# Kernel tuning notes

Measured on AMD Instinct MI355X. Metric: run time of the kernel, lower is better.

Reference implementation:

```python
import jax, jax.numpy as jnp
import numpy as np

BN_EPS = 1e-5


def setup_inputs() -> dict:
    key = jax.random.key(0)
    k1, k2, k3, k4 = jax.random.split(key, 4)
    N_IN, N_OUT, K, M, C_IN, C_OUT = 500000, 125000, 27, 60000, 64, 64
    x = jax.random.normal(k1, (N_IN, C_IN), dtype=jnp.float32)
    # Per-offset conv weights, fan-in scaled like Minkowski's kaiming init
    W = jax.random.normal(k2, (K, C_IN, C_OUT), dtype=jnp.float32) * (1.0 / np.sqrt(K * C_IN))
    gamma = jnp.ones((C_OUT,), dtype=jnp.float32)
    beta = jnp.zeros((C_OUT,), dtype=jnp.float32)
    # Kernel map: for each of the 27 offsets, M (input_idx, output_idx) pairs
    in_idx = jax.random.randint(k3, (K, M), 0, N_IN, dtype=jnp.int64)
    out_idx = jax.random.randint(k4, (K, M), 0, N_OUT, dtype=jnp.int64)
    return {"x": x, "W": W, "gamma": gamma, "beta": beta,
            "in_idx": in_idx, "out_idx": out_idx, "n_out": 125000}


def reference(x, W, gamma, beta, in_idx, out_idx, n_out):
    # Sparse 3D conv via kernel map: gather -> per-offset GEMM -> scatter-add.
    C_out = W.shape[-1]
    gathered = x[in_idx]                                   # [K, M, C_in]
    contrib = jnp.einsum('kmc,kcd->kmd', gathered, W)      # [K, M, C_out]
    out = jnp.zeros((n_out, C_out), dtype=x.dtype)
    out = out.at[out_idx.reshape(-1)].add(contrib.reshape(-1, C_out))  # [N_out, C_out]
    # MinkowskiBatchNorm (training mode): per-channel batch stats over all points
    mean = jnp.mean(out, axis=0)
    var = jnp.mean(jnp.square(out - mean), axis=0)         # biased variance
    y = (out - mean) * jax.lax.rsqrt(var + BN_EPS) * gamma + beta
    return y
```

## Files before the change

kernel.cpp:

```cpp
#include <hip/hip_runtime.h>

typedef __attribute__((ext_vector_type(8))) short short8;
typedef __attribute__((ext_vector_type(4))) float f32x4;

#define K_OFF    27
#define M_PAIRS  60000
#define C_DIM    64
#define N_IN     500000
#define N_OUT_C  125000
#define BN_EPS   1e-5f
#define E_TOT    (K_OFF * M_PAIRS)

#define TILES_PER_K  ((M_PAIRS + 63) / 64)
#define TOTAL_WT     (K_OFF * TILES_PER_K)

#define CONTRIB_BYTES ((size_t)E_TOT * C_DIM * 2)
#define WT_OFF    CONTRIB_BYTES
#define WT_BYTES  ((size_t)K_OFF * C_DIM * C_DIM * 2)
#define CNT_OFF   (WT_OFF + WT_BYTES)
#define CNT_BYTES ((size_t)N_OUT_C * 4)
#define OFF_OFF   (CNT_OFF + CNT_BYTES)
#define CUR_OFF   (OFF_OFF + CNT_BYTES)
#define BSUM_OFF  (CUR_OFF + CNT_BYTES)
#define ST_OFF    (BSUM_OFF + 4096)
#define XB_OFF    ((ST_OFF + 512 + 255) & ~(size_t)255)
#define XB_BYTES  ((size_t)N_IN * C_DIM * 2)
#define WS_MID    XB_OFF
#define WS_FULL   (XB_OFF + XB_BYTES)

#define SCAN_BS 256
#define SCAN_NB ((N_OUT_C + SCAN_BS - 1) / SCAN_BS)

#define PREP_XBLK 2048
#define PREP_WBLK ((K_OFF * C_DIM * C_DIM + 255) / 256)
#define PREP_HBLK 1024

__device__ __forceinline__ unsigned short f32_to_bf16(float f) {
    unsigned u = __float_as_uint(f);
    u += 0x7FFFu + ((u >> 16) & 1u);
    return (unsigned short)(u >> 16);
}
__device__ __forceinline__ float bf16f(unsigned short u) {
    return __uint_as_float((unsigned)u << 16);
}

__global__ __launch_bounds__(256) void prep(
    const float* __restrict__ x, unsigned short* __restrict__ xb,
    const float* __restrict__ W, unsigned short* __restrict__ wt,
    const int* __restrict__ out_idx, unsigned* __restrict__ cnt, int nx)
{
    int b = blockIdx.x;
    if (b < nx) {
        const int tid = b * 256 + threadIdx.x;
        const int T   = nx * 256;
        const int n4  = N_IN * C_DIM / 4;
        const float4* x4 = (const float4*)x;
        ushort4* b4 = (ushort4*)xb;
        for (int i = tid; i < n4; i += T) {
            float4 v = x4[i];
            ushort4 o;
            o.x = f32_to_bf16(v.x); o.y = f32_to_bf16(v.y);
            o.z = f32_to_bf16(v.z); o.w = f32_to_bf16(v.w);
            b4[i] = o;
        }
        return;
    }
    b -= nx;
    if (b < PREP_WBLK) {
        const int tid = b * 256 + threadIdx.x;
        if (tid < K_OFF * C_DIM * C_DIM) {
            const int c = tid & 63;
            const int d = (tid >> 6) & 63;
            const int k = tid >> 12;
            wt[tid] = f32_to_bf16(W[(k << 12) + (c << 6) + d]);
        }
        return;
    }
    b -= PREP_WBLK;
    for (int e = b * 256 + threadIdx.x; e < E_TOT; e += PREP_HBLK * 256)
        atomicAdd(&cnt[out_idx[e]], 1u);
}

__global__ __launch_bounds__(SCAN_BS) void scan_a(const unsigned* __restrict__ cnt,
                                                  unsigned* __restrict__ off,
                                                  unsigned* __restrict__ bsum) {
    __shared__ unsigned s[SCAN_BS];
    const int idx = blockIdx.x * SCAN_BS + threadIdx.x;
    const unsigned v = (idx < N_OUT_C) ? cnt[idx] : 0u;
    s[threadIdx.x] = v;
    __syncthreads();
    for (int d = 1; d < SCAN_BS; d <<= 1) {
        unsigned t = (threadIdx.x >= d) ? s[threadIdx.x - d] : 0u;
        __syncthreads();
        s[threadIdx.x] += t;
        __syncthreads();
    }
    if (idx < N_OUT_C) off[idx] = s[threadIdx.x] - v;
    if (threadIdx.x == SCAN_BS - 1) bsum[blockIdx.x] = s[threadIdx.x];
}

__global__ __launch_bounds__(512) void scan_b(unsigned* __restrict__ bsum) {
    __shared__ unsigned s[512];
    const unsigned v = (threadIdx.x < SCAN_NB) ? bsum[threadIdx.x] : 0u;
    s[threadIdx.x] = v;
    __syncthreads();
    for (int d = 1; d < 512; d <<= 1) {
        unsigned t = (threadIdx.x >= d) ? s[threadIdx.x - d] : 0u;
        __syncthreads();
        s[threadIdx.x] += t;
        __syncthreads();
    }
    if (threadIdx.x < SCAN_NB) bsum[threadIdx.x] = s[threadIdx.x] - v;
}

__global__ __launch_bounds__(SCAN_BS) void scan_c(unsigned* __restrict__ off,
                                                  unsigned* __restrict__ cur,
                                                  const unsigned* __restrict__ bsum) {
    const int idx = blockIdx.x * SCAN_BS + threadIdx.x;
    if (idx < N_OUT_C) {
        const unsigned o = off[idx] + bsum[blockIdx.x];
        off[idx] = o;
        cur[idx] = o;
    }
}

template<bool BF16G>
__global__ __launch_bounds__(256, 4) void mfma_contrib(
    const float* __restrict__ x, const unsigned short* __restrict__ xb,
    const unsigned short* __restrict__ wt,
    const int* __restrict__ in_idx, const int* __restrict__ out_idx,
    unsigned* __restrict__ cursor, unsigned short* __restrict__ contrib)
{
    const int gwave = blockIdx.x * 4 + (threadIdx.x >> 6);
    if (gwave >= TOTAL_WT) return;
    const int lane = threadIdx.x & 63;
    const int lg = lane >> 4;
    const int lr = lane & 15;

    const int k  = gwave / TILES_PER_K;
    const int t  = gwave % TILES_PER_K;
    const int m0 = t * 64;
    const int kbase = k * M_PAIRS;

    short8 bfr[2][4];
    const unsigned short* wtk = wt + (size_t)k * C_DIM * C_DIM;
#pragma unroll
    for (int ks = 0; ks < 2; ++ks)
#pragma unroll
        for (int ct = 0; ct < 4; ++ct)
            bfr[ks][ct] = *(const short8*)(wtk + (ct * 16 + lr) * C_DIM + ks * 32 + lg * 8);

    int pos = -1;
    {
        const int mrow = m0 + lane;
        if (mrow < M_PAIRS)
            pos = (int)atomicAdd(&cursor[out_idx[kbase + mrow]], 1u);
    }

    int aidx[4];
#pragma unroll
    for (int rt = 0; rt < 4; ++rt) {
        const int m = m0 + rt * 16 + lr;
        aidx[rt] = (m < M_PAIRS) ? in_idx[kbase + m] : -1;
    }

    f32x4 acc[4][4] = {};
#pragma unroll
    for (int ks = 0; ks < 2; ++ks) {
#pragma unroll
        for (int rt = 0; rt < 4; ++rt) {
            short8 a = {};
            if (aidx[rt] >= 0) {
                if constexpr (BF16G) {
                    a = *(const short8*)(xb + (size_t)aidx[rt] * C_DIM + ks * 32 + lg * 8);
                } else {
                    const float* xr = x + (size_t)aidx[rt] * C_DIM + ks * 32 + lg * 8;
                    float4 f0 = *(const float4*)xr;
                    float4 f1 = *(const float4*)(xr + 4);
                    a[0] = (short)f32_to_bf16(f0.x); a[1] = (short)f32_to_bf16(f0.y);
                    a[2] = (short)f32_to_bf16(f0.z); a[3] = (short)f32_to_bf16(f0.w);
                    a[4] = (short)f32_to_bf16(f1.x); a[5] = (short)f32_to_bf16(f1.y);
                    a[6] = (short)f32_to_bf16(f1.z); a[7] = (short)f32_to_bf16(f1.w);
                }
            }
#pragma unroll
            for (int ct = 0; ct < 4; ++ct)
                acc[rt][ct] = __builtin_amdgcn_mfma_f32_16x16x32_bf16(
                    a, bfr[ks][ct], acc[rt][ct], 0, 0, 0);
        }
    }

#pragma unroll
    for (int rt = 0; rt < 4; ++rt) {
#pragma unroll
        for (int j = 0; j < 4; ++j) {
            const int r = rt * 16 + lg * 4 + j;
            const int p = __shfl(pos, r);
            if (p >= 0) {
                unsigned short* dst = contrib + (size_t)p * C_DIM + lr;
#pragma unroll
                for (int ct = 0; ct < 4; ++ct)
                    dst[ct * 16] = f32_to_bf16(acc[rt][ct][j]);
            }
        }
    }
}

__global__ __launch_bounds__(256) void reduce_bn(
    const unsigned short* __restrict__ contrib, const unsigned* __restrict__ off,
    const unsigned* __restrict__ cnt, float* __restrict__ out,
    float* __restrict__ stats)
{
    __shared__ float ls[128];
    if (threadIdx.x < 128) ls[threadIdx.x] = 0.f;
    __syncthreads();
    const int lane = threadIdx.x & 63;
    const int lg = lane >> 4;
    const int lr = lane & 15;
    const int wid  = blockIdx.x * 4 + (threadIdx.x >> 6);
    const int NW   = gridDim.x * 4;
    const int span = (N_OUT_C + NW - 1) / NW;
    const int o0 = wid * span;
    const int o1 = (o0 + span < N_OUT_C) ? o0 + span : N_OUT_C;

    float ts0 = 0, ts1 = 0, ts2 = 0, ts3 = 0;
    float tq0 = 0, tq1 = 0, tq2 = 0, tq3 = 0;
    for (int o = o0; o < o1; ++o) {
        const unsigned base = off[o];
        const int n = (int)cnt[o];
        float s0 = 0, s1 = 0, s2 = 0, s3 = 0;
        for (int i = lg; i < n; i += 4) {
            const ushort4 u = *(const ushort4*)(
                contrib + ((size_t)base + i) * C_DIM + lr * 4);
            s0 += bf16f(u.x); s1 += bf16f(u.y);
            s2 += bf16f(u.z); s3 += bf16f(u.w);
        }
        s0 += __shfl_xor(s0, 16); s1 += __shfl_xor(s1, 16);
        s2 += __shfl_xor(s2, 16); s3 += __shfl_xor(s3, 16);
        s0 += __shfl_xor(s0, 32); s1 += __shfl_xor(s1, 32);
        s2 += __shfl_xor(s2, 32); s3 += __shfl_xor(s3, 32);
        if (lg == 0) {
            *(float4*)(out + (size_t)o * C_DIM + lr * 4) =
                make_float4(s0, s1, s2, s3);
            ts0 += s0; tq0 = fmaf(s0, s0, tq0);
            ts1 += s1; tq1 = fmaf(s1, s1, tq1);
            ts2 += s2; tq2 = fmaf(s2, s2, tq2);
            ts3 += s3; tq3 = fmaf(s3, s3, tq3);
        }
    }
    if (lg == 0) {
        atomicAdd(&ls[lr * 4 + 0], ts0); atomicAdd(&ls[lr * 4 + 1], ts1);
        atomicAdd(&ls[lr * 4 + 2], ts2); atomicAdd(&ls[lr * 4 + 3], ts3);
        atomicAdd(&ls[64 + lr * 4 + 0], tq0); atomicAdd(&ls[64 + lr * 4 + 1], tq1);
        atomicAdd(&ls[64 + lr * 4 + 2], tq2); atomicAdd(&ls[64 + lr * 4 + 3], tq3);
    }
    __syncthreads();
    if (threadIdx.x < 128) unsafeAtomicAdd(&stats[threadIdx.x], ls[threadIdx.x]);
}

__global__ __launch_bounds__(256) void bn_apply_f32(
    float* __restrict__ out, const float* __restrict__ stats,
    const float* __restrict__ gamma, const float* __restrict__ beta)
{
    __shared__ float ssc[C_DIM], ssh[C_DIM];
    if (threadIdx.x < C_DIM) {
        const float inv_n = 1.0f / (float)N_OUT_C;
        float mean = stats[threadIdx.x] * inv_n;
        float var  = stats[C_DIM + threadIdx.x] * inv_n - mean * mean;
        float inv  = rsqrtf(var + BN_EPS);
        float s    = inv * gamma[threadIdx.x];
        ssc[threadIdx.x] = s;
        ssh[threadIdx.x] = beta[threadIdx.x] - mean * s;
    }
    __syncthreads();
    const int tid = blockIdx.x * blockDim.x + threadIdx.x;
    const int T   = gridDim.x * blockDim.x;
    const int cq  = (tid & 15) * 4;
    const int total4 = N_OUT_C * C_DIM / 4;
    const float4 sc = make_float4(ssc[cq], ssc[cq+1], ssc[cq+2], ssc[cq+3]);
    const float4 sh = make_float4(ssh[cq], ssh[cq+1], ssh[cq+2], ssh[cq+3]);
    float4* o4 = (float4*)out;
    for (int i = tid; i < total4; i += T) {
        float4 v = o4[i];
        v.x = fmaf(v.x, sc.x, sh.x);
        v.y = fmaf(v.y, sc.y, sh.y);
        v.z = fmaf(v.z, sc.z, sh.z);
        v.w = fmaf(v.w, sc.w, sh.w);
        o4[i] = v;
    }
}

#define FCHUNKS  37
#define FWPK     (FCHUNKS * 4)
#define FSPAN    ((M_PAIRS + FWPK - 1) / FWPK)

__global__ __launch_bounds__(256, 4) void conv_scatter(
    const float* __restrict__ x, const float* __restrict__ W,
    const int* __restrict__ in_idx, const int* __restrict__ out_idx,
    float* __restrict__ out)
{
    const int k     = blockIdx.x / FCHUNKS;
    const int chunk = blockIdx.x % FCHUNKS;
    const int wid   = chunk * 4 + (threadIdx.x >> 6);
    const int lane  = threadIdx.x & 63;
    float wcol[C_DIM];
    const float* Wk = W + (size_t)k * C_DIM * C_DIM;
#pragma unroll
    for (int c = 0; c < C_DIM; ++c) wcol[c] = Wk[c * C_DIM + lane];
    const int kbase = k * M_PAIRS;
    const int m0 = wid * FSPAN;
    const int m1 = (m0 + FSPAN < M_PAIRS) ? m0 + FSPAN : M_PAIRS;
    for (int m = m0; m < m1; ++m) {
        int ii = __builtin_amdgcn_readfirstlane(in_idx[kbase + m]);
        int oi = __builtin_amdgcn_readfirstlane(out_idx[kbase + m]);
        const float* xr = x + (size_t)ii * C_DIM;
        float a0=0.f,a1=0.f,a2=0.f,a3=0.f;
#pragma unroll
        for (int c = 0; c < C_DIM; c += 4) {
            a0 = fmaf(xr[c+0], wcol[c+0], a0);
            a1 = fmaf(xr[c+1], wcol[c+1], a1);
            a2 = fmaf(xr[c+2], wcol[c+2], a2);
            a3 = fmaf(xr[c+3], wcol[c+3], a3);
        }
        unsafeAtomicAdd(out + (size_t)oi * C_DIM + lane, (a0+a1)+(a2+a3));
    }
}

__global__ __launch_bounds__(256) void bn_stats_f32(
    const float* __restrict__ acc, float* __restrict__ stats)
{
    const int tid = blockIdx.x * blockDim.x + threadIdx.x;
    const int T   = gridDim.x * blockDim.x;
    const int cq  = (tid & 15) * 4;
    const int total4 = N_OUT_C * C_DIM / 4;
    float s0=0,s1=0,s2=0,s3=0,q0=0,q1=0,q2=0,q3=0;
    const float4* a4 = (const float4*)acc;
    for (int i = tid; i < total4; i += T) {
        float4 v = a4[i];
        s0+=v.x; q0=fmaf(v.x,v.x,q0);
        s1+=v.y; q1=fmaf(v.y,v.y,q1);
        s2+=v.z; q2=fmaf(v.z,v.z,q2);
        s3+=v.w; q3=fmaf(v.w,v.w,q3);
    }
    __shared__ float ls[128];
    if (threadIdx.x < 128) ls[threadIdx.x] = 0.f;
    __syncthreads();
    atomicAdd(&ls[cq+0],s0); atomicAdd(&ls[cq+1],s1);
    atomicAdd(&ls[cq+2],s2); atomicAdd(&ls[cq+3],s3);
    atomicAdd(&ls[64+cq+0],q0); atomicAdd(&ls[64+cq+1],q1);
    atomicAdd(&ls[64+cq+2],q2); atomicAdd(&ls[64+cq+3],q3);
    __syncthreads();
    if (threadIdx.x < 128) unsafeAtomicAdd(&stats[threadIdx.x], ls[threadIdx.x]);
}

extern "C" void kernel_launch(void* const* d_in, const int* in_sizes, int n_in,
                              void* d_out, int out_size, void* d_ws, size_t ws_size,
                              hipStream_t stream)
{
    const float* x       = (const float*)d_in[0];
    const float* W       = (const float*)d_in[1];
    const float* gamma   = (const float*)d_in[2];
    const float* beta    = (const float*)d_in[3];
    const int*   in_idx  = (const int*)d_in[4];
    const int*   out_idx = (const int*)d_in[5];
    float* out = (float*)d_out;

    if (ws_size >= WS_MID) {
        unsigned short* contrib = (unsigned short*)d_ws;
        unsigned short* wt      = (unsigned short*)((char*)d_ws + WT_OFF);
        unsigned* cnt           = (unsigned*)((char*)d_ws + CNT_OFF);
        unsigned* off           = (unsigned*)((char*)d_ws + OFF_OFF);
        unsigned* cur           = (unsigned*)((char*)d_ws + CUR_OFF);
        unsigned* bsum          = (unsigned*)((char*)d_ws + BSUM_OFF);
        float* stats            = (float*)((char*)d_ws + ST_OFF);
        unsigned short* xb      = (unsigned short*)((char*)d_ws + XB_OFF);
        const bool full         = (ws_size >= WS_FULL);
        const int nx            = full ? PREP_XBLK : 0;

        hipMemsetAsync(cnt, 0, CNT_BYTES, stream);
        hipMemsetAsync(stats, 0, 128 * sizeof(float), stream);
        prep<<<nx + PREP_WBLK + PREP_HBLK, 256, 0, stream>>>(
            x, xb, W, wt, out_idx, cnt, nx);
        scan_a<<<SCAN_NB, SCAN_BS, 0, stream>>>(cnt, off, bsum);
        scan_b<<<1, 512, 0, stream>>>(bsum);
        scan_c<<<SCAN_NB, SCAN_BS, 0, stream>>>(off, cur, bsum);
        if (full)
            mfma_contrib<true><<<(TOTAL_WT + 3) / 4, 256, 0, stream>>>(
                x, xb, wt, in_idx, out_idx, cur, contrib);
        else
            mfma_contrib<false><<<(TOTAL_WT + 3) / 4, 256, 0, stream>>>(
                x, xb, wt, in_idx, out_idx, cur, contrib);
        reduce_bn<<<2048, 256, 0, stream>>>(contrib, off, cnt, out, stats);
        bn_apply_f32<<<1024, 256, 0, stream>>>(out, stats, gamma, beta);
    } else {
        float* stats = (float*)d_ws;
        hipMemsetAsync(out, 0, (size_t)N_OUT_C * C_DIM * sizeof(float), stream);
        hipMemsetAsync(stats, 0, 128 * sizeof(float), stream);
        conv_scatter<<<K_OFF * FCHUNKS, 256, 0, stream>>>(x, W, in_idx, out_idx, out);
        bn_stats_f32<<<512, 256, 0, stream>>>(out, stats);
        bn_apply_f32<<<1024, 256, 0, stream>>>(out, stats, gamma, beta);
    }
}
```

Baseline: 394.3 us.

## Record per-edge rank in histogram pass to skip cursor atomics in GEMM

```diff
diff --git a/kernel.cpp b/kernel.cpp
--- a/kernel.cpp
+++ b/kernel.cpp
@@ -2,6 +2,7 @@
 
 typedef __attribute__((ext_vector_type(8))) short short8;
 typedef __attribute__((ext_vector_type(4))) float f32x4;
+typedef __attribute__((ext_vector_type(4))) unsigned short us4;
 
 #define K_OFF    27
 #define M_PAIRS  60000
@@ -25,8 +26,11 @@
 #define ST_OFF    (BSUM_OFF + 4096)
 #define XB_OFF    ((ST_OFF + 512 + 255) & ~(size_t)255)
 #define XB_BYTES  ((size_t)N_IN * C_DIM * 2)
+#define POS_BYTES ((size_t)E_TOT * 4)
 #define WS_MID    XB_OFF
+#define WS_T3     (XB_OFF + POS_BYTES)
 #define WS_FULL   (XB_OFF + XB_BYTES)
+#define WS_T1     (XB_OFF + XB_BYTES + POS_BYTES)
 
 #define SCAN_BS 256
 #define SCAN_NB ((N_OUT_C + SCAN_BS - 1) / SCAN_BS)
@@ -47,18 +51,19 @@
 __global__ __launch_bounds__(256) void prep(
     const float* __restrict__ x, unsigned short* __restrict__ xb,
     const float* __restrict__ W, unsigned short* __restrict__ wt,
-    const int* __restrict__ out_idx, unsigned* __restrict__ cnt, int nx)
+    const int* __restrict__ out_idx, unsigned* __restrict__ cnt,
+    unsigned* __restrict__ pos, int nx)
 {
     int b = blockIdx.x;
     if (b < nx) {
         const int tid = b * 256 + threadIdx.x;
         const int T   = nx * 256;
         const int n4  = N_IN * C_DIM / 4;
-        const float4* x4 = (const float4*)x;
-        ushort4* b4 = (ushort4*)xb;
+        const f32x4* x4 = (const f32x4*)x;
+        us4* b4 = (us4*)xb;
         for (int i = tid; i < n4; i += T) {
-            float4 v = x4[i];
-            ushort4 o;
+            f32x4 v = __builtin_nontemporal_load(&x4[i]);
+            us4 o;
             o.x = f32_to_bf16(v.x); o.y = f32_to_bf16(v.y);
             o.z = f32_to_bf16(v.z); o.w = f32_to_bf16(v.w);
             b4[i] = o;
@@ -77,8 +82,13 @@
         return;
     }
     b -= PREP_WBLK;
-    for (int e = b * 256 + threadIdx.x; e < E_TOT; e += PREP_HBLK * 256)
-        atomicAdd(&cnt[out_idx[e]], 1u);
+    if (pos) {
+        for (int e = b * 256 + threadIdx.x; e < E_TOT; e += PREP_HBLK * 256)
+            pos[e] = atomicAdd(&cnt[out_idx[e]], 1u);
+    } else {
+        for (int e = b * 256 + threadIdx.x; e < E_TOT; e += PREP_HBLK * 256)
+            atomicAdd(&cnt[out_idx[e]], 1u);
+    }
 }
 
 __global__ __launch_bounds__(SCAN_BS) void scan_a(const unsigned* __restrict__ cnt,
@@ -124,12 +134,13 @@
     }
 }
 
-template<bool BF16G>
+template<bool BF16G, bool RANKED>
 __global__ __launch_bounds__(256, 4) void mfma_contrib(
     const float* __restrict__ x, const unsigned short* __restrict__ xb,
     const unsigned short* __restrict__ wt,
     const int* __restrict__ in_idx, const int* __restrict__ out_idx,
-    unsigned* __restrict__ cursor, unsigned short* __restrict__ contrib)
+    const unsigned* __restrict__ offf, unsigned* __restrict__ cursor,
+    const unsigned* __restrict__ pos_local, unsigned short* __restrict__ contrib)
 {
     const int gwave = blockIdx.x * 4 + (threadIdx.x >> 6);
     if (gwave >= TOTAL_WT) return;
@@ -153,8 +164,13 @@
     int pos = -1;
     {
         const int mrow = m0 + lane;
-        if (mrow < M_PAIRS)
-            pos = (int)atomicAdd(&cursor[out_idx[kbase + mrow]], 1u);
+        if (mrow < M_PAIRS) {
+            const int e = kbase + mrow;
+            if constexpr (RANKED)
+                pos = (int)(offf[out_idx[e]] + pos_local[e]);
+            else
+                pos = (int)atomicAdd(&cursor[out_idx[e]], 1u);
+        }
     }
 
     int aidx[4];
@@ -230,8 +246,8 @@
         const int n = (int)cnt[o];
         float s0 = 0, s1 = 0, s2 = 0, s3 = 0;
         for (int i = lg; i < n; i += 4) {
-            const ushort4 u = *(const ushort4*)(
-                contrib + ((size_t)base + i) * C_DIM + lr * 4);
+            const us4 u = __builtin_nontemporal_load(
+                (const us4*)(contrib + ((size_t)base + i) * C_DIM + lr * 4));
             s0 += bf16f(u.x); s1 += bf16f(u.y);
             s2 += bf16f(u.z); s3 += bf16f(u.w);
         }
@@ -259,6 +275,98 @@
 }
 
 __global__ __launch_bounds__(256) void bn_apply_f32(
+    float* __restrict__ out, const float* __restrict__ stats,
+    const float* __restrict__ gamma, const float* __restrict__ beta)
+{
+    __shared__ float ssc[C_DIM], ssh[C_DIM];
+    if (threadIdx.x < C_DIM) {
+        const float inv_n = 1.0f / (float)N_OUT_C;
+        float mean = stats[threadIdx.x] * inv_n;
+        float var  = stats[C_DIM + threadIdx.x] * inv_n - mean * mean;
+        float inv  = rsqrtf(var + BN_EPS);
+        float s    = inv * gamma[threadIdx.x];
+        ssc[threadIdx.x] = s;
+        ssh[threadIdx.x] = beta[threadIdx.x] - mean * s;
+    }
+    __syncthreads();
+    const int tid = blockIdx.x * blockDim.x + threadIdx.x;
+    const int T   = gridDim.x * blockDim.x;
+    const int cq  = (tid & 15) * 4;
+    const int total4 = N_OUT_C * C_DIM / 4;
+    const f32x4 sc = {ssc[cq], ssc[cq+1], ssc[cq+2], ssc[cq+3]};
+    const f32x4 sh = {ssh[cq], ssh[cq+1], ssh[cq+2], ssh[cq+3]};
+    f32x4* o4 = (f32x4*)out;
+    for (int i = tid; i < total4; i += T) {
+        f32x4 v = o4[i];
+        v = v * sc + sh;
+        __builtin_nontemporal_store(v, &o4[i]);
+    }
+}
+
+#define FCHUNKS  37
+#define FWPK     (FCHUNKS * 4)
+#define FSPAN    ((M_PAIRS + FWPK - 1) / FWPK)
+
+__global__ __launch_bounds__(256, 4) void conv_scatter(
+    const float* __restrict__ x, const float* __restrict__ W,
+    const int* __restrict__ in_idx, const int* __restrict__ out_idx,
+    float* __restrict__ out)
+{
+    const int k     = blockIdx.x / FCHUNKS;
+    const int chunk = blockIdx.x % FCHUNKS;
+    const int wid   = chunk * 4 + (threadIdx.x >> 6);
+    const int lane  = threadIdx.x & 63;
+    float wcol[C_DIM];
+    const float* Wk = W + (size_t)k * C_DIM * C_DIM;
+#pragma unroll
+    for (int c = 0; c < C_DIM; ++c) wcol[c] = Wk[c * C_DIM + lane];
+    const int kbase = k * M_PAIRS;
+    const int m0 = wid * FSPAN;
+    const int m1 = (m0 + FSPAN < M_PAIRS) ? m0 + FSPAN : M_PAIRS;
+    for (int m = m0; m < m1; ++m) {
+        int ii = __builtin_amdgcn_readfirstlane(in_idx[kbase + m]);
+        int oi = __builtin_amdgcn_readfirstlane(out_idx[kbase + m]);
+        const float* xr = x + (size_t)ii * C_DIM;
+        float a0=0.f,a1=0.f,a2=0.f,a3=0.f;
+#pragma unroll
+        for (int c = 0; c < C_DIM; c += 4) {
+            a0 = fmaf(xr[c+0], wcol[c+0], a0);
+            a1 = fmaf(xr[c+1], wcol[c+1], a1);
+            a2 = fmaf(xr[c+2], wcol[c+2], a2);
+            a3 = fmaf(xr[c+3], wcol[c+3], a3);
+        }
+        unsafeAtomicAdd(out + (size_t)oi * C_DIM + lane, (a0+a1)+(a2+a3));
+    }
+}
+
+__global__ __launch_bounds__(256) void bn_stats_f32(
+    const float* __restrict__ acc, float* __restrict__ stats)
+{
+    const int tid = blockIdx.x * blockDim.x + threadIdx.x;
+    const int T   = gridDim.x * blockDim.x;
+    const int cq  = (tid & 15) * 4;
+    const int total4 = N_OUT_C * C_DIM / 4;
+    float s0=0,s1=0,s2=0,s3=0,q0=0,q1=0,q2=0,q3=0;
+    const float4* a4 = (const float4*)acc;
+    for (int i = tid; i < total4; i += T) {
+        float4 v = a4[i];
+        s0+=v.x; q0=fmaf(v.x,v.x,q0);
+        s1+=v.y; q1=fmaf(v.y,v.y,q1);
+        s2+=v.z; q2=fmaf(v.z,v.z,q2);
+        s3+=v.w; q3=fmaf(v.w,v.w,q3);
+    }
+    __shared__ float ls[128];
+    if (threadIdx.x < 128) ls[threadIdx.x] = 0.f;
+    __syncthreads();
+    atomicAdd(&ls[cq+0],s0); atomicAdd(&ls[cq+1],s1);
+    atomicAdd(&ls[cq+2],s2); atomicAdd(&ls[cq+3],s3);
+    atomicAdd(&ls[64+cq+0],q0); atomicAdd(&ls[64+cq+1],q1);
+    atomicAdd(&ls[64+cq+2],q2); atomicAdd(&ls[64+cq+3],q3);
+    __syncthreads();
+    if (threadIdx.x < 128) unsafeAtomicAdd(&stats[threadIdx.x], ls[threadIdx.x]);
+}
+
+__global__ __launch_bounds__(256) void bn_apply_fb(
     float* __restrict__ out, const float* __restrict__ stats,
     const float* __restrict__ gamma, const float* __restrict__ beta)
 {
@@ -290,69 +398,6 @@
     }
 }
 
-#define FCHUNKS  37
-#define FWPK     (FCHUNKS * 4)
-#define FSPAN    ((M_PAIRS + FWPK - 1) / FWPK)
-
-__global__ __launch_bounds__(256, 4) void conv_scatter(
-    const float* __restrict__ x, const float* __restrict__ W,
-    const int* __restrict__ in_idx, const int* __restrict__ out_idx,
-    float* __restrict__ out)
-{
-    const int k     = blockIdx.x / FCHUNKS;
-    const int chunk = blockIdx.x % FCHUNKS;
-    const int wid   = chunk * 4 + (threadIdx.x >> 6);
-    const int lane  = threadIdx.x & 63;
-    float wcol[C_DIM];
-    const float* Wk = W + (size_t)k * C_DIM * C_DIM;
-#pragma unroll
-    for (int c = 0; c < C_DIM; ++c) wcol[c] = Wk[c * C_DIM + lane];
-    const int kbase = k * M_PAIRS;
-    const int m0 = wid * FSPAN;
-    const int m1 = (m0 + FSPAN < M_PAIRS) ? m0 + FSPAN : M_PAIRS;
-    for (int m = m0; m < m1; ++m) {
-        int ii = __builtin_amdgcn_readfirstlane(in_idx[kbase + m]);
-        int oi = __builtin_amdgcn_readfirstlane(out_idx[kbase + m]);
-        const float* xr = x + (size_t)ii * C_DIM;
-        float a0=0.f,a1=0.f,a2=0.f,a3=0.f;
-#pragma unroll
-        for (int c = 0; c < C_DIM; c += 4) {
-            a0 = fmaf(xr[c+0], wcol[c+0], a0);
-            a1 = fmaf(xr[c+1], wcol[c+1], a1);
-            a2 = fmaf(xr[c+2], wcol[c+2], a2);
-            a3 = fmaf(xr[c+3], wcol[c+3], a3);
-        }
-        unsafeAtomicAdd(out + (size_t)oi * C_DIM + lane, (a0+a1)+(a2+a3));
-    }
-}
-
-__global__ __launch_bounds__(256) void bn_stats_f32(
-    const float* __restrict__ acc, float* __restrict__ stats)
-{
-    const int tid = blockIdx.x * blockDim.x + threadIdx.x;
-    const int T   = gridDim.x * blockDim.x;
-    const int cq  = (tid & 15) * 4;
-    const int total4 = N_OUT_C * C_DIM / 4;
-    float s0=0,s1=0,s2=0,s3=0,q0=0,q1=0,q2=0,q3=0;
-    const float4* a4 = (const float4*)acc;
-    for (int i = tid; i < total4; i += T) {
-        float4 v = a4[i];
-        s0+=v.x; q0=fmaf(v.x,v.x,q0);
-        s1+=v.y; q1=fmaf(v.y,v.y,q1);
-        s2+=v.z; q2=fmaf(v.z,v.z,q2);
-        s3+=v.w; q3=fmaf(v.w,v.w,q3);
-    }
-    __shared__ float ls[128];
-    if (threadIdx.x < 128) ls[threadIdx.x] = 0.f;
-    __syncthreads();
-    atomicAdd(&ls[cq+0],s0); atomicAdd(&ls[cq+1],s1);
-    atomicAdd(&ls[cq+2],s2); atomicAdd(&ls[cq+3],s3);
-    atomicAdd(&ls[64+cq+0],q0); atomicAdd(&ls[64+cq+1],q1);
-    atomicAdd(&ls[64+cq+2],q2); atomicAdd(&ls[64+cq+3],q3);
-    __syncthreads();
-    if (threadIdx.x < 128) unsafeAtomicAdd(&stats[threadIdx.x], ls[threadIdx.x]);
-}
-
 extern "C" void kernel_launch(void* const* d_in, const int* in_sizes, int n_in,
                               void* d_out, int out_size, void* d_ws, size_t ws_size,
                               hipStream_t stream)
@@ -374,23 +419,37 @@
         unsigned* bsum          = (unsigned*)((char*)d_ws + BSUM_OFF);
         float* stats            = (float*)((char*)d_ws + ST_OFF);
         unsigned short* xb      = (unsigned short*)((char*)d_ws + XB_OFF);
-        const bool full         = (ws_size >= WS_FULL);
-        const int nx            = full ? PREP_XBLK : 0;
+
+        const bool full   = (ws_size >= WS_FULL);
+        const bool ranked = full ? (ws_size >= WS_T1) : (ws_size >= WS_T3);
+        unsigned* pos = ranked
+            ? (unsigned*)((char*)d_ws + (full ? (XB_OFF + XB_BYTES) : XB_OFF))
+            : nullptr;
+        const int nx = full ? PREP_XBLK : 0;
 
         hipMemsetAsync(cnt, 0, CNT_BYTES, stream);
         hipMemsetAsync(stats, 0, 128 * sizeof(float), stream);
         prep<<<nx + PREP_WBLK + PREP_HBLK, 256, 0, stream>>>(
-            x, xb, W, wt, out_idx, cnt, nx);
+            x, xb, W, wt, out_idx, cnt, pos, nx);
         scan_a<<<SCAN_NB, SCAN_BS, 0, stream>>>(cnt, off, bsum);
         scan_b<<<1, 512, 0, stream>>>(bsum);
         scan_c<<<SCAN_NB, SCAN_BS, 0, stream>>>(off, cur, bsum);
-        if (full)
-            mfma_contrib<true><<<(TOTAL_WT + 3) / 4, 256, 0, stream>>>(
-                x, xb, wt, in_idx, out_idx, cur, contrib);
+
+        const int cgrid = (TOTAL_WT + 3) / 4;
+        if (full && ranked)
+            mfma_contrib<true, true><<<cgrid, 256, 0, stream>>>(
+                x, xb, wt, in_idx, out_idx, off, cur, pos, contrib);
+        else if (full)
+            mfma_contrib<true, false><<<cgrid, 256, 0, stream>>>(
+                x, xb, wt, in_idx, out_idx, off, cur, pos, contrib);
+        else if (ranked)
+            mfma_contrib<false, true><<<cgrid, 256, 0, stream>>>(
+                x, xb, wt, in_idx, out_idx, off, cur, pos, contrib);
         else
-            mfma_contrib<false><<<(TOTAL_WT + 3) / 4, 256, 0, stream>>>(
-                x, xb, wt, in_idx, out_idx, cur, contrib);
-        reduce_bn<<<2048, 256, 0, stream>>>(contrib, off, cnt, out, stats);
+            mfma_contrib<false, false><<<cgrid, 256, 0, stream>>>(
+                x, xb, wt, in_idx, out_idx, off, cur, pos, contrib);
+
+        reduce_bn<<<4096, 256, 0, stream>>>(contrib, off, cnt, out, stats);
         bn_apply_f32<<<1024, 256, 0, stream>>>(out, stats, gamma, beta);
     } else {
         float* stats = (float*)d_ws;
@@ -398,6 +457,6 @@
         hipMemsetAsync(stats, 0, 128 * sizeof(float), stream);
         conv_scatter<<<K_OFF * FCHUNKS, 256, 0, stream>>>(x, W, in_idx, out_idx, out);
         bn_stats_f32<<<512, 256, 0, stream>>>(out, stats);
-        bn_apply_f32<<<1024, 256, 0, stream>>>(out, stats, gamma, beta);
-    }
-}
+        bn_apply_fb<<<1024, 256, 0, stream>>>(out, stats, gamma, beta);
+    }
+}
```

Measured after the change: 408.2 us. 1.04x slower.
